# Performance work log

Hardware: AMD Instinct MI355X
Metric: run time of the kernel (lower is better)

The kernel has to match this reference:

```python
import jax, jax.numpy as jnp
import numpy as np


def _gelu(x):
    # torch nn.GELU default = exact erf form
    return jax.nn.gelu(x, approximate=False)


def setup_inputs() -> dict:
    key = jax.random.key(0)
    ks = jax.random.split(key, 10)
    B, C, S, L, Din, Dout = 32, 4, 256, 256, 256, 256
    return {
        "features": jax.random.normal(ks[0], (B, C, S, Din), jnp.float32),
        "features_mean": jax.random.normal(ks[1], (B, S, L), jnp.float32),
        "W1": jax.random.normal(ks[2], (1, 16), jnp.float32) * 0.5,
        "b1": jax.random.normal(ks[3], (16,), jnp.float32) * 0.1,
        "W2": jax.random.normal(ks[4], (16, 8), jnp.float32) * 0.25,
        "b2": jax.random.normal(ks[5], (8,), jnp.float32) * 0.1,
        "W3": jax.random.normal(ks[6], (8, 2), jnp.float32) * 0.35,
        "b3": jax.random.normal(ks[7], (2,), jnp.float32) * 0.1,
        "Wl": jax.random.normal(ks[8], (Din, Dout), jnp.float32) * (1.0 / np.sqrt(Din)),
        "bl": jax.random.normal(ks[9], (Dout,), jnp.float32) * 0.02,
    }


def reference(features, features_mean, W1, b1, W2, b2, W3, b3, Wl, bl):
    B, S, L = features_mean.shape
    # pairwise correlations -> [B, S*S, 1]
    corr = jnp.einsum('bsl,btl->bst', features_mean, features_mean).reshape(B, S * S, 1)
    # tiny pointwise MLP 1->16->8->2 with GELU, then log-softmax
    h = _gelu(corr @ W1 + b1)
    h = _gelu(h @ W2 + b2)
    logits = jax.nn.log_softmax(h @ W3 + b3, axis=-1)  # [B, S*S, 2]
    # gumbel-softmax, hard=True, tau=1 (straight-through; forward value is one-hot)
    u = jax.random.uniform(jax.random.key(42), logits.shape, logits.dtype, 1e-10, 1.0)
    g = -jnp.log(-jnp.log(u))
    y_soft = jax.nn.softmax(logits + g, axis=-1)
    y_hard = jax.nn.one_hot(jnp.argmax(y_soft, axis=-1), 2, dtype=y_soft.dtype)
    y = jax.lax.stop_gradient(y_hard - y_soft) + y_soft
    adj = y[..., 0].reshape(B, S, S)
    # mix in identity: a + (1 - a) * I (forces self-loops)
    eye = jnp.eye(S, dtype=adj.dtype)
    adj = adj + (1.0 - adj) * eye
    # degree (row) normalization
    adj = adj * (1.0 / jnp.sum(adj, axis=-1, keepdims=True))
    # propagate: [B,1,S,S] @ [B,C,S,Din]
    x = jnp.einsum('bst,bctd->bcsd', adj, features)
    return x @ Wl + bl
```

## Files before the change

### kernel.cpp

```cpp
#include <hip/hip_runtime.h>
#include <stdint.h>


#define TBL_INTERVALS 131072
#define TBL_MIN -128.0f
#define TBL_SCALE 512.0f
#define WL_CAP 131072u

typedef __attribute__((ext_vector_type(8))) short short8v;
typedef __attribute__((ext_vector_type(4))) short short4v;
typedef __attribute__((ext_vector_type(4))) float float4v;

__device__ __forceinline__ void threefry2x32(uint32_t x0, uint32_t x1,
                                             uint32_t& o0, uint32_t& o1) {
  const uint32_t ks0 = 0u;
  const uint32_t ks1 = 42u;
  const uint32_t ks2 = 0x1BD11BDAu ^ ks0 ^ ks1;
  const uint32_t ks[3] = {ks0, ks1, ks2};
  const uint32_t rot[2][4] = {{13u, 15u, 26u, 6u}, {17u, 29u, 16u, 24u}};
  x0 += ks0;
  x1 += ks1;
#pragma unroll
  for (int i = 0; i < 5; ++i) {
#pragma unroll
    for (int j = 0; j < 4; ++j) {
      const uint32_t r = rot[i & 1][j];
      x0 += x1;
      x1 = (x1 << r) | (x1 >> (32u - r));
      x1 ^= x0;
    }
    x0 += ks[(i + 1) % 3];
    x1 += ks[(i + 2) % 3] + (uint32_t)(i + 1);
  }
  o0 = x0;
  o1 = x1;
}

__device__ __forceinline__ float uniform_at(uint32_t j) {
  uint32_t o0, o1;
  threefry2x32(0u, j, o0, o1);
  const uint32_t bits = o0 ^ o1;
  uint32_t fb = (bits >> 9) | 0x3F800000u;
  float frac = __uint_as_float(fb) - 1.0f;
  return fmaxf(frac + 1e-10f, 1e-10f);
}

__device__ __forceinline__ double gumbel64_at(uint32_t j) {
  double t = -log((double)uniform_at(j));
  return -log(t);
}

__device__ __forceinline__ float gumbel32_at(uint32_t j) {
  float t = -logf(uniform_at(j));
  return -logf(t);
}

__device__ __forceinline__ double gelu_d(double x) {
  return 0.5 * x * (1.0 + erf(x * 0.70710678118654752440));
}

__device__ __forceinline__ float gelu_f(float x) {
  return 0.5f * x * (1.0f + erff(x * 0.70710678f));
}

__device__ __forceinline__ float mlp32(float corr, const float* __restrict__ W1,
                                       const float* __restrict__ b1,
                                       const float* __restrict__ W2,
                                       const float* __restrict__ b2,
                                       const float* __restrict__ W3,
                                       const float* __restrict__ b3) {
  float h1[16];
#pragma unroll
  for (int u = 0; u < 16; ++u) h1[u] = gelu_f(fmaf(corr, W1[u], b1[u]));
  float h2[8];
#pragma unroll
  for (int v = 0; v < 8; ++v) {
    float x = b2[v];
#pragma unroll
    for (int u = 0; u < 16; ++u) x = fmaf(h1[u], W2[u * 8 + v], x);
    h2[v] = gelu_f(x);
  }
  float l0 = b3[0], l1 = b3[1];
#pragma unroll
  for (int v = 0; v < 8; ++v) {
    l0 = fmaf(h2[v], W3[v * 2 + 0], l0);
    l1 = fmaf(h2[v], W3[v * 2 + 1], l1);
  }
  return l0 - l1;
}

__device__ __forceinline__ void split_bf16(float x, short& h, short& l) {
  uint32_t u = __float_as_uint(x);
  uint32_t hr = (u + 0x7FFFu + ((u >> 16) & 1u)) >> 16;
  float hf = __uint_as_float(hr << 16);
  float lo = x - hf;
  uint32_t v = __float_as_uint(lo);
  uint32_t lr = (v + 0x7FFFu + ((v >> 16) & 1u)) >> 16;
  h = (short)hr;
  l = (short)lr;
}

__global__ __launch_bounds__(256) void build_table_kernel(
    const float* __restrict__ W1, const float* __restrict__ b1,
    const float* __restrict__ W2, const float* __restrict__ b2,
    const float* __restrict__ W3, const float* __restrict__ b3,
    float* __restrict__ tbl, uint32_t* __restrict__ counter) {
  const int i = blockIdx.x * 256 + threadIdx.x;
  if (i == 0) counter[0] = 0u;
  if (i > TBL_INTERVALS) return;
  const float x = TBL_MIN + (float)i * (1.0f / TBL_SCALE);
  tbl[i] = mlp32(x, W1, b1, W2, b2, W3, b3);
}

__global__ __launch_bounds__(256) void corr_mfma_kernel(
    const float* __restrict__ fm, float* __restrict__ corr) {
  const int b = blockIdx.z;
  const float* base = fm + (size_t)b * 65536;
  const int row0 = blockIdx.y * 128;
  const int col0 = blockIdx.x * 128;

  __shared__ short Ah[128][40];
  __shared__ short Al[128][40];
  __shared__ short Bh[128][40];
  __shared__ short Bl[128][40];

  const int tid = threadIdx.x;
  const int w = tid >> 6;
  const int wr = (w >> 1) * 64;
  const int wc = (w & 1) * 64;
  const int lane = tid & 63;
  const int fcol = lane & 15;
  const int kg = lane >> 4;

  const int am = tid >> 1;
  const int ak = (tid & 1) * 16;

  float4v acc[4][4];
#pragma unroll
  for (int i = 0; i < 4; ++i)
#pragma unroll
    for (int j = 0; j < 4; ++j) acc[i][j] = (float4v)(0.0f);

  for (int k0 = 0; k0 < 256; k0 += 32) {
    float4 av[4], bv[4];
#pragma unroll
    for (int q = 0; q < 4; ++q) {
      av[q] = *(const float4*)(base + (size_t)(row0 + am) * 256 + k0 + ak + q * 4);
      bv[q] = *(const float4*)(base + (size_t)(col0 + am) * 256 + k0 + ak + q * 4);
    }

    __syncthreads();

    {
      short h[16], l[16];
#pragma unroll
      for (int q = 0; q < 4; ++q) {
        split_bf16(av[q].x, h[q * 4 + 0], l[q * 4 + 0]);
        split_bf16(av[q].y, h[q * 4 + 1], l[q * 4 + 1]);
        split_bf16(av[q].z, h[q * 4 + 2], l[q * 4 + 2]);
        split_bf16(av[q].w, h[q * 4 + 3], l[q * 4 + 3]);
      }
      *(short8v*)&Ah[am][ak] = *(short8v*)&h[0];
      *(short8v*)&Ah[am][ak + 8] = *(short8v*)&h[8];
      *(short8v*)&Al[am][ak] = *(short8v*)&l[0];
      *(short8v*)&Al[am][ak + 8] = *(short8v*)&l[8];
#pragma unroll
      for (int q = 0; q < 4; ++q) {
        split_bf16(bv[q].x, h[q * 4 + 0], l[q * 4 + 0]);
        split_bf16(bv[q].y, h[q * 4 + 1], l[q * 4 + 1]);
        split_bf16(bv[q].z, h[q * 4 + 2], l[q * 4 + 2]);
        split_bf16(bv[q].w, h[q * 4 + 3], l[q * 4 + 3]);
      }
      *(short8v*)&Bh[am][ak] = *(short8v*)&h[0];
      *(short8v*)&Bh[am][ak + 8] = *(short8v*)&h[8];
      *(short8v*)&Bl[am][ak] = *(short8v*)&l[0];
      *(short8v*)&Bl[am][ak + 8] = *(short8v*)&l[8];
    }
    __syncthreads();

    short8v afh[4], afl[4], bfh[4], bfl[4];
#pragma unroll
    for (int im = 0; im < 4; ++im) {
      afh[im] = *(const short8v*)&Ah[wr + im * 16 + fcol][kg * 8];
      afl[im] = *(const short8v*)&Al[wr + im * 16 + fcol][kg * 8];
    }
#pragma unroll
    for (int in = 0; in < 4; ++in) {
      bfh[in] = *(const short8v*)&Bh[wc + in * 16 + fcol][kg * 8];
      bfl[in] = *(const short8v*)&Bl[wc + in * 16 + fcol][kg * 8];
    }
#pragma unroll
    for (int im = 0; im < 4; ++im)
#pragma unroll
      for (int in = 0; in < 4; ++in) {
        acc[im][in] = __builtin_amdgcn_mfma_f32_16x16x32_bf16(
            afh[im], bfh[in], acc[im][in], 0, 0, 0);
        acc[im][in] = __builtin_amdgcn_mfma_f32_16x16x32_bf16(
            afh[im], bfl[in], acc[im][in], 0, 0, 0);
        acc[im][in] = __builtin_amdgcn_mfma_f32_16x16x32_bf16(
            afl[im], bfh[in], acc[im][in], 0, 0, 0);
        acc[im][in] = __builtin_amdgcn_mfma_f32_16x16x32_bf16(
            afl[im], bfl[in], acc[im][in], 0, 0, 0);
      }
  }

  float* Cb = corr + (size_t)b * 65536;
#pragma unroll
  for (int in = 0; in < 4; ++in) {
    const int col = col0 + wc + in * 16 + fcol;
#pragma unroll
    for (int im = 0; im < 4; ++im) {
      const int rbase = row0 + wr + im * 16 + kg * 4;
#pragma unroll
      for (int r = 0; r < 4; ++r)
        Cb[(size_t)(rbase + r) * 256 + col] = acc[im][in][r];
    }
  }
}

__global__ __launch_bounds__(256) void decide_fast_kernel(
    const float* __restrict__ corr, const float* __restrict__ tbl,
    unsigned short* __restrict__ adj_bin, uint32_t* __restrict__ counter,
    uint32_t* __restrict__ worklist, float* __restrict__ rowsumF) {
  const uint32_t flat = blockIdx.x * 256u + threadIdx.x;
  const int t = threadIdx.x;
  const int s = blockIdx.x & 255;

  float a = 1.0f;
  bool pend = false;
  if (t != s) {
    const float cf = corr[flat];
    if (fabsf(cf) >= 127.0f) {
      pend = true;
      a = 0.0f;
    } else {
      const float xf = (cf - TBL_MIN) * TBL_SCALE;
      const int i = (int)xf;
      const float fr = xf - (float)i;
      const float t0v = tbl[i];
      const float t1v = tbl[i + 1];
      const float dt = t1v - t0v;
      const float dphi = fmaf(fr, dt, t0v);

      const float g0 = gumbel32_at(2u * flat);
      const float g1 = gumbel32_at(2u * flat + 1u);
      const float d = dphi - (g1 - g0);
      const float thr = fmaf(fabsf(dt), 0.3072f, 4e-4f);
      if (fabsf(d) >= thr) {
        a = (d >= 0.0f) ? 1.0f : 0.0f;
      } else {
        pend = true;
        a = 0.0f;
      }
    }
  }
  if (pend) {
    const uint32_t idx = atomicAdd(counter, 1u);
    if (idx < WL_CAP) worklist[idx] = flat;
  }
  adj_bin[flat] = (a == 1.0f) ? (unsigned short)0x3F80u : (unsigned short)0u;

  float sum = a;
#pragma unroll
  for (int off = 32; off; off >>= 1) sum += __shfl_xor(sum, off);
  __shared__ float red[4];
  if ((threadIdx.x & 63) == 0) red[threadIdx.x >> 6] = sum;
  __syncthreads();
  if (threadIdx.x == 0)
    rowsumF[blockIdx.x] = red[0] + red[1] + red[2] + red[3];
}

__global__ __launch_bounds__(256) void decide_exact_kernel(
    const float* __restrict__ fm, const uint32_t* __restrict__ counter,
    const uint32_t* __restrict__ worklist,
    const float* __restrict__ W1, const float* __restrict__ b1,
    const float* __restrict__ W2, const float* __restrict__ b2,
    const float* __restrict__ W3, const float* __restrict__ b3,
    unsigned short* __restrict__ adj_bin, float* __restrict__ rowsumF) {
  const uint32_t n = min(counter[0], WL_CAP);
  const uint32_t waveId = (blockIdx.x * 256u + threadIdx.x) >> 6;
  const uint32_t nWaves = (gridDim.x * 256u) >> 6;
  const int lane = threadIdx.x & 63;

  for (uint32_t it = waveId; it < n; it += nWaves) {
    const uint32_t flat = worklist[it];
    const uint32_t bb = flat >> 16;
    const uint32_t ss = (flat >> 8) & 255u;
    const uint32_t tt = flat & 255u;

    const float* S = fm + ((size_t)bb * 256 + ss) * 256;
    const float* T = fm + ((size_t)bb * 256 + tt) * 256;
    double p = 0.0;
#pragma unroll
    for (int q = 0; q < 4; ++q) {
      const int k = lane + q * 64;
      p += (double)S[k] * (double)T[k];
    }
#pragma unroll
    for (int off = 32; off; off >>= 1) p += __shfl_xor(p, off);
    const double acc = p;

    const double ga = gumbel64_at(2u * flat + (uint32_t)(lane & 1));

    const int u = lane & 15;
    const double h1 = gelu_d(acc * (double)W1[u] + (double)b1[u]);

    const int v = lane & 7;
    double sv = (double)b2[v];
#pragma unroll
    for (int uu = 0; uu < 16; ++uu) {
      const double h1u = __shfl(h1, uu);
      sv += h1u * (double)W2[uu * 8 + v];
    }
    const double h2 = gelu_d(sv);

    double l0 = (double)b3[0], l1 = (double)b3[1];
#pragma unroll
    for (int vv = 0; vv < 8; ++vv) {
      const double h2v = __shfl(h2, vv);
      l0 += h2v * (double)W3[vv * 2 + 0];
      l1 += h2v * (double)W3[vv * 2 + 1];
    }

    const double G0 = __shfl(ga, 0);
    const double G1 = __shfl(ga, 1);
    if (lane == 0) {
      const bool one = (l0 + G0 >= l1 + G1);
      adj_bin[flat] = one ? (unsigned short)0x3F80u : (unsigned short)0u;
      if (one) atomicAdd(&rowsumF[flat >> 8], 1.0f);
    }
  }
}

__global__ __launch_bounds__(256) void gemm_binA_kernel(
    const unsigned short* __restrict__ A, const float* __restrict__ B,
    const float* __restrict__ rowsumF, float* __restrict__ C) {
  const int z = blockIdx.z;
  const unsigned short* Ab = A + (size_t)(z / 4) * 65536;
  const float* Bb = B + (size_t)z * 65536;
  const float* rsb = rowsumF + (size_t)(z / 4) * 256;
  float* Cb = C + (size_t)z * 65536;

  const int row0 = blockIdx.y * 128;
  const int col0 = blockIdx.x * 128;

  __shared__ short Ah[128][40];
  __shared__ short Bh[128][40];
  __shared__ short Bl[128][40];

  const int tid = threadIdx.x;
  const int w = tid >> 6;
  const int wr = (w >> 1) * 64;
  const int wc = (w & 1) * 64;
  const int lane = tid & 63;
  const int fcol = lane & 15;
  const int kg = lane >> 4;

  const int am = tid >> 1;
  const int ak = (tid & 1) * 16;
  const int nq = (tid & 31) * 4;
  const int kb = (tid >> 5) * 4;

  float4v acc[4][4];
#pragma unroll
  for (int i = 0; i < 4; ++i)
#pragma unroll
    for (int j = 0; j < 4; ++j) acc[i][j] = (float4v)(0.0f);

  for (int k0 = 0; k0 < 256; k0 += 32) {
    short8v a0 = *(const short8v*)(Ab + (size_t)(row0 + am) * 256 + k0 + ak);
    short8v a1 = *(const short8v*)(Ab + (size_t)(row0 + am) * 256 + k0 + ak + 8);
    float4 bv[4];
#pragma unroll
    for (int j = 0; j < 4; ++j)
      bv[j] = *(const float4*)(Bb + (size_t)(k0 + kb + j) * 256 + col0 + nq);

    __syncthreads();

    *(short8v*)&Ah[am][ak] = a0;
    *(short8v*)&Ah[am][ak + 8] = a1;
    {
      const float bm[4][4] = {{bv[0].x, bv[1].x, bv[2].x, bv[3].x},
                              {bv[0].y, bv[1].y, bv[2].y, bv[3].y},
                              {bv[0].z, bv[1].z, bv[2].z, bv[3].z},
                              {bv[0].w, bv[1].w, bv[2].w, bv[3].w}};
#pragma unroll
      for (int i = 0; i < 4; ++i) {
        short h[4], l[4];
#pragma unroll
        for (int j = 0; j < 4; ++j) split_bf16(bm[i][j], h[j], l[j]);
        *(short4v*)&Bh[nq + i][kb] = *(short4v*)&h[0];
        *(short4v*)&Bl[nq + i][kb] = *(short4v*)&l[0];
      }
    }
    __syncthreads();

    short8v afh[4], bfh[4], bfl[4];
#pragma unroll
    for (int im = 0; im < 4; ++im)
      afh[im] = *(const short8v*)&Ah[wr + im * 16 + fcol][kg * 8];
#pragma unroll
    for (int in = 0; in < 4; ++in) {
      bfh[in] = *(const short8v*)&Bh[wc + in * 16 + fcol][kg * 8];
      bfl[in] = *(const short8v*)&Bl[wc + in * 16 + fcol][kg * 8];
    }
#pragma unroll
    for (int im = 0; im < 4; ++im)
#pragma unroll
      for (int in = 0; in < 4; ++in) {
        acc[im][in] = __builtin_amdgcn_mfma_f32_16x16x32_bf16(
            afh[im], bfh[in], acc[im][in], 0, 0, 0);
        acc[im][in] = __builtin_amdgcn_mfma_f32_16x16x32_bf16(
            afh[im], bfl[in], acc[im][in], 0, 0, 0);
      }
  }

#pragma unroll
  for (int im = 0; im < 4; ++im) {
    const int rbase = row0 + wr + im * 16 + kg * 4;
    float rsv[4];
#pragma unroll
    for (int r = 0; r < 4; ++r) rsv[r] = 1.0f / rsb[rbase + r];
#pragma unroll
    for (int in = 0; in < 4; ++in) {
      const int col = col0 + wc + in * 16 + fcol;
#pragma unroll
      for (int r = 0; r < 4; ++r)
        Cb[(size_t)(rbase + r) * 256 + col] = acc[im][in][r] * rsv[r];
    }
  }
}

__global__ __launch_bounds__(256) void gemm_mfma_kernel(
    const float* __restrict__ A, const float* __restrict__ B,
    const float* __restrict__ bias, float* __restrict__ C) {
  const int z = blockIdx.z;
  const float* Ab = A + (size_t)z * 65536;
  const float* Bb = B;
  float* Cb = C + (size_t)z * 65536;

  const int row0 = blockIdx.y * 128;
  const int col0 = blockIdx.x * 128;

  __shared__ short Ah[128][40];
  __shared__ short Al[128][40];
  __shared__ short Bh[128][40];
  __shared__ short Bl[128][40];

  const int tid = threadIdx.x;
  const int w = tid >> 6;
  const int wr = (w >> 1) * 64;
  const int wc = (w & 1) * 64;
  const int lane = tid & 63;
  const int fcol = lane & 15;
  const int kg = lane >> 4;

  const int am = tid >> 1;
  const int ak = (tid & 1) * 16;
  const int nq = (tid & 31) * 4;
  const int kb = (tid >> 5) * 4;

  float4v acc[4][4];
#pragma unroll
  for (int i = 0; i < 4; ++i)
#pragma unroll
    for (int j = 0; j < 4; ++j) acc[i][j] = (float4v)(0.0f);

  for (int k0 = 0; k0 < 256; k0 += 32) {
    float4 av[4];
#pragma unroll
    for (int q = 0; q < 4; ++q)
      av[q] = *(const float4*)(Ab + (size_t)(row0 + am) * 256 + k0 + ak + q * 4);
    float4 bv[4];
#pragma unroll
    for (int j = 0; j < 4; ++j)
      bv[j] = *(const float4*)(Bb + (size_t)(k0 + kb + j) * 256 + col0 + nq);

    __syncthreads();

    {
      short h[16], l[16];
#pragma unroll
      for (int q = 0; q < 4; ++q) {
        split_bf16(av[q].x, h[q * 4 + 0], l[q * 4 + 0]);
        split_bf16(av[q].y, h[q * 4 + 1], l[q * 4 + 1]);
        split_bf16(av[q].z, h[q * 4 + 2], l[q * 4 + 2]);
        split_bf16(av[q].w, h[q * 4 + 3], l[q * 4 + 3]);
      }
      *(short8v*)&Ah[am][ak] = *(short8v*)&h[0];
      *(short8v*)&Ah[am][ak + 8] = *(short8v*)&h[8];
      *(short8v*)&Al[am][ak] = *(short8v*)&l[0];
      *(short8v*)&Al[am][ak + 8] = *(short8v*)&l[8];
    }
    {
      const float bm[4][4] = {{bv[0].x, bv[1].x, bv[2].x, bv[3].x},
                              {bv[0].y, bv[1].y, bv[2].y, bv[3].y},
                              {bv[0].z, bv[1].z, bv[2].z, bv[3].z},
                              {bv[0].w, bv[1].w, bv[2].w, bv[3].w}};
#pragma unroll
      for (int i = 0; i < 4; ++i) {
        short h[4], l[4];
#pragma unroll
        for (int j = 0; j < 4; ++j) split_bf16(bm[i][j], h[j], l[j]);
        *(short4v*)&Bh[nq + i][kb] = *(short4v*)&h[0];
        *(short4v*)&Bl[nq + i][kb] = *(short4v*)&l[0];
      }
    }
    __syncthreads();

    short8v afh[4], afl[4], bfh[4], bfl[4];
#pragma unroll
    for (int im = 0; im < 4; ++im) {
      afh[im] = *(const short8v*)&Ah[wr + im * 16 + fcol][kg * 8];
      afl[im] = *(const short8v*)&Al[wr + im * 16 + fcol][kg * 8];
    }
#pragma unroll
    for (int in = 0; in < 4; ++in) {
      bfh[in] = *(const short8v*)&Bh[wc + in * 16 + fcol][kg * 8];
      bfl[in] = *(const short8v*)&Bl[wc + in * 16 + fcol][kg * 8];
    }
#pragma unroll
    for (int im = 0; im < 4; ++im)
#pragma unroll
      for (int in = 0; in < 4; ++in) {
        acc[im][in] = __builtin_amdgcn_mfma_f32_16x16x32_bf16(
            afh[im], bfh[in], acc[im][in], 0, 0, 0);
        acc[im][in] = __builtin_amdgcn_mfma_f32_16x16x32_bf16(
            afh[im], bfl[in], acc[im][in], 0, 0, 0);
        acc[im][in] = __builtin_amdgcn_mfma_f32_16x16x32_bf16(
            afl[im], bfh[in], acc[im][in], 0, 0, 0);
      }
  }

#pragma unroll
  for (int in = 0; in < 4; ++in) {
    const int col = col0 + wc + in * 16 + fcol;
    const float bvx = bias[col];
#pragma unroll
    for (int im = 0; im < 4; ++im) {
      const int rbase = row0 + wr + im * 16 + kg * 4;
#pragma unroll
      for (int r = 0; r < 4; ++r)
        Cb[(size_t)(rbase + r) * 256 + col] = acc[im][in][r] + bvx;
    }
  }
}

extern "C" void kernel_launch(void* const* d_in, const int* in_sizes, int n_in,
                              void* d_out, int out_size, void* d_ws,
                              size_t ws_size, hipStream_t stream) {
  const float* features = (const float*)d_in[0];
  const float* fm       = (const float*)d_in[1];
  const float* W1 = (const float*)d_in[2];
  const float* b1 = (const float*)d_in[3];
  const float* W2 = (const float*)d_in[4];
  const float* b2 = (const float*)d_in[5];
  const float* W3 = (const float*)d_in[6];
  const float* b3 = (const float*)d_in[7];
  const float* Wl = (const float*)d_in[8];
  const float* bl = (const float*)d_in[9];
  float* out = (float*)d_out;

  char* ws = (char*)d_ws;
  float* tbl          = (float*)ws;
  float* rowsumF      = (float*)(ws + 576u * 1024u);
  uint32_t* counter   = (uint32_t*)(ws + 640u * 1024u);
  uint32_t* worklist  = counter + 16;
  unsigned short* adj = (unsigned short*)(ws + 2u * 1024u * 1024u);
  float* corr         = (float*)(ws + 10800u * 1024u);
  float* X            = (float*)(ws + 10800u * 1024u);

  build_table_kernel<<<dim3(513), 256, 0, stream>>>(W1, b1, W2, b2, W3, b3,
                                                    tbl, counter);
  corr_mfma_kernel<<<dim3(2, 2, 32), 256, 0, stream>>>(fm, corr);
  decide_fast_kernel<<<dim3(8192), 256, 0, stream>>>(corr, tbl, adj, counter,
                                                     worklist, rowsumF);
  decide_exact_kernel<<<dim3(2048), 256, 0, stream>>>(fm, counter, worklist,
                                                      W1, b1, W2, b2, W3, b3,
                                                      adj, rowsumF);
  gemm_binA_kernel<<<dim3(2, 2, 128), 256, 0, stream>>>(adj, features,
                                                        rowsumF, X);
  gemm_mfma_kernel<<<dim3(2, 2, 128), 256, 0, stream>>>(X, Wl, bl, out);
}
```

Measured before the change: 94.08 us.

## Fuse adjacency propagation GEMM with output linear GEMM; merge table build into corr kernel

Replaces the two back-to-back GEMM kernels with one kernel. Each block computes a 32-row strip of adj@features, keeps the normalized result in LDS as a bf16 hi/lo pair, then multiplies it by Wl, so the intermediate X never goes to global memory. The table-build kernel is also folded into the correlation kernel as extra blocks, which removes one launch. In exchange each block needs about 73KB of dynamic LDS, which lowers occupancy. The smaller 32-row tiles also mean every block re-reads full feature and Wl panels, adding redundant global traffic and repeated bf16 splitting.

```diff
diff --git a/kernel.cpp b/kernel.cpp
--- a/kernel.cpp
+++ b/kernel.cpp
@@ -6,6 +6,7 @@
 #define TBL_MIN -128.0f
 #define TBL_SCALE 512.0f
 #define WL_CAP 131072u
+#define FUSED_LDS 74752
 
 typedef __attribute__((ext_vector_type(8))) short short8v;
 typedef __attribute__((ext_vector_type(4))) short short4v;
@@ -100,24 +101,27 @@
   l = (short)lr;
 }
 
-__global__ __launch_bounds__(256) void build_table_kernel(
+__global__ __launch_bounds__(256) void corr_table_kernel(
+    const float* __restrict__ fm, float* __restrict__ corr,
     const float* __restrict__ W1, const float* __restrict__ b1,
     const float* __restrict__ W2, const float* __restrict__ b2,
     const float* __restrict__ W3, const float* __restrict__ b3,
     float* __restrict__ tbl, uint32_t* __restrict__ counter) {
-  const int i = blockIdx.x * 256 + threadIdx.x;
-  if (i == 0) counter[0] = 0u;
-  if (i > TBL_INTERVALS) return;
-  const float x = TBL_MIN + (float)i * (1.0f / TBL_SCALE);
-  tbl[i] = mlp32(x, W1, b1, W2, b2, W3, b3);
-}
-
-__global__ __launch_bounds__(256) void corr_mfma_kernel(
-    const float* __restrict__ fm, float* __restrict__ corr) {
-  const int b = blockIdx.z;
+  if (blockIdx.x >= 128) {
+    const int i = (int)(blockIdx.x - 128) * 256 + threadIdx.x;
+    if (blockIdx.x == 128 && threadIdx.x == 0) counter[0] = 0u;
+    if (i <= TBL_INTERVALS) {
+      const float x = TBL_MIN + (float)i * (1.0f / TBL_SCALE);
+      tbl[i] = mlp32(x, W1, b1, W2, b2, W3, b3);
+    }
+    return;
+  }
+
+  const int bid = blockIdx.x;
+  const int b = bid >> 2;
+  const int row0 = ((bid >> 1) & 1) * 128;
+  const int col0 = (bid & 1) * 128;
   const float* base = fm + (size_t)b * 65536;
-  const int row0 = blockIdx.y * 128;
-  const int col0 = blockIdx.x * 128;
 
   __shared__ short Ah[128][40];
   __shared__ short Al[128][40];
@@ -332,216 +336,184 @@
   }
 }
 
-__global__ __launch_bounds__(256) void gemm_binA_kernel(
-    const unsigned short* __restrict__ A, const float* __restrict__ B,
-    const float* __restrict__ rowsumF, float* __restrict__ C) {
-  const int z = blockIdx.z;
-  const unsigned short* Ab = A + (size_t)(z / 4) * 65536;
-  const float* Bb = B + (size_t)z * 65536;
-  const float* rsb = rowsumF + (size_t)(z / 4) * 256;
-  float* Cb = C + (size_t)z * 65536;
-
-  const int row0 = blockIdx.y * 128;
-  const int col0 = blockIdx.x * 128;
-
-  __shared__ short Ah[128][40];
-  __shared__ short Bh[128][40];
-  __shared__ short Bl[128][40];
+__global__ __launch_bounds__(256) void fused_out_kernel(
+    const unsigned short* __restrict__ adjp, const float* __restrict__ F,
+    const float* __restrict__ Wl, const float* __restrict__ bl,
+    const float* __restrict__ rowsumF, float* __restrict__ out) {
+  extern __shared__ char smem[];
+  short* Aadj = (short*)smem;
+  short* Xh = (short*)smem;
+  short* Xl = Xh + 32 * 264;
+  short* Bh = (short*)(smem + 33792);
+  short* Bl = Bh + 256 * 40;
+
+  const int bid = blockIdx.x;
+  const int z = bid & 127;
+  const int rg = bid >> 7;
+  const int b = z >> 2;
+  const int row0 = rg * 32;
+
+  const unsigned short* Ab = adjp + (size_t)b * 65536 + (size_t)row0 * 256;
+  const float* Fb = F + (size_t)z * 65536;
+  const float* rsb = rowsumF + b * 256 + row0;
+  float* Ob = out + (size_t)z * 65536 + (size_t)row0 * 256;
 
   const int tid = threadIdx.x;
   const int w = tid >> 6;
-  const int wr = (w >> 1) * 64;
-  const int wc = (w & 1) * 64;
+  const int wc2 = w * 64;
   const int lane = tid & 63;
   const int fcol = lane & 15;
   const int kg = lane >> 4;
 
-  const int am = tid >> 1;
-  const int ak = (tid & 1) * 16;
-  const int nq = (tid & 31) * 4;
+  const int nq = (tid & 31) * 8;
   const int kb = (tid >> 5) * 4;
 
-  float4v acc[4][4];
-#pragma unroll
-  for (int i = 0; i < 4; ++i)
+  {
+    const int r = tid >> 3;
+    const int c0 = (tid & 7) * 32;
+#pragma unroll
+    for (int q = 0; q < 4; ++q) {
+      short8v v = *(const short8v*)(Ab + (size_t)r * 256 + c0 + q * 8);
+      *(short8v*)&Aadj[r * 264 + c0 + q * 8] = v;
+    }
+  }
+
+  float4v acc[2][4];
+#pragma unroll
+  for (int i = 0; i < 2; ++i)
 #pragma unroll
     for (int j = 0; j < 4; ++j) acc[i][j] = (float4v)(0.0f);
 
   for (int k0 = 0; k0 < 256; k0 += 32) {
-    short8v a0 = *(const short8v*)(Ab + (size_t)(row0 + am) * 256 + k0 + ak);
-    short8v a1 = *(const short8v*)(Ab + (size_t)(row0 + am) * 256 + k0 + ak + 8);
-    float4 bv[4];
-#pragma unroll
-    for (int j = 0; j < 4; ++j)
-      bv[j] = *(const float4*)(Bb + (size_t)(k0 + kb + j) * 256 + col0 + nq);
-
+    float4 bv[4][2];
+#pragma unroll
+    for (int j = 0; j < 4; ++j) {
+      bv[j][0] = *(const float4*)(Fb + (size_t)(k0 + kb + j) * 256 + nq);
+      bv[j][1] = *(const float4*)(Fb + (size_t)(k0 + kb + j) * 256 + nq + 4);
+    }
     __syncthreads();
-
-    *(short8v*)&Ah[am][ak] = a0;
-    *(short8v*)&Ah[am][ak + 8] = a1;
-    {
-      const float bm[4][4] = {{bv[0].x, bv[1].x, bv[2].x, bv[3].x},
-                              {bv[0].y, bv[1].y, bv[2].y, bv[3].y},
-                              {bv[0].z, bv[1].z, bv[2].z, bv[3].z},
-                              {bv[0].w, bv[1].w, bv[2].w, bv[3].w}};
-#pragma unroll
-      for (int i = 0; i < 4; ++i) {
-        short h[4], l[4];
-#pragma unroll
-        for (int j = 0; j < 4; ++j) split_bf16(bm[i][j], h[j], l[j]);
-        *(short4v*)&Bh[nq + i][kb] = *(short4v*)&h[0];
-        *(short4v*)&Bl[nq + i][kb] = *(short4v*)&l[0];
-      }
+#pragma unroll
+    for (int i = 0; i < 8; ++i) {
+      short h[4], l[4];
+#pragma unroll
+      for (int j = 0; j < 4; ++j) {
+        const float4& f = bv[j][i >> 2];
+        const float x = ((i & 3) == 0) ? f.x
+                       : ((i & 3) == 1) ? f.y
+                       : ((i & 3) == 2) ? f.z : f.w;
+        split_bf16(x, h[j], l[j]);
+      }
+      *(short4v*)&Bh[(nq + i) * 40 + kb] = *(short4v*)&h[0];
+      *(short4v*)&Bl[(nq + i) * 40 + kb] = *(short4v*)&l[0];
     }
     __syncthreads();
 
-    short8v afh[4], bfh[4], bfl[4];
-#pragma unroll
-    for (int im = 0; im < 4; ++im)
-      afh[im] = *(const short8v*)&Ah[wr + im * 16 + fcol][kg * 8];
+    short8v af[2], bfh[4], bfl[4];
+#pragma unroll
+    for (int im = 0; im < 2; ++im)
+      af[im] = *(const short8v*)&Aadj[(im * 16 + fcol) * 264 + k0 + kg * 8];
 #pragma unroll
     for (int in = 0; in < 4; ++in) {
-      bfh[in] = *(const short8v*)&Bh[wc + in * 16 + fcol][kg * 8];
-      bfl[in] = *(const short8v*)&Bl[wc + in * 16 + fcol][kg * 8];
-    }
-#pragma unroll
-    for (int im = 0; im < 4; ++im)
+      bfh[in] = *(const short8v*)&Bh[(wc2 + in * 16 + fcol) * 40 + kg * 8];
+      bfl[in] = *(const short8v*)&Bl[(wc2 + in * 16 + fcol) * 40 + kg * 8];
+    }
+#pragma unroll
+    for (int im = 0; im < 2; ++im)
 #pragma unroll
       for (int in = 0; in < 4; ++in) {
         acc[im][in] = __builtin_amdgcn_mfma_f32_16x16x32_bf16(
+            af[im], bfh[in], acc[im][in], 0, 0, 0);
+        acc[im][in] = __builtin_amdgcn_mfma_f32_16x16x32_bf16(
+            af[im], bfl[in], acc[im][in], 0, 0, 0);
+      }
+  }
+
+  __syncthreads();
+  {
+    float rsv[2][4];
+#pragma unroll
+    for (int im = 0; im < 2; ++im)
+#pragma unroll
+      for (int r = 0; r < 4; ++r)
+        rsv[im][r] = 1.0f / rsb[im * 16 + kg * 4 + r];
+#pragma unroll
+    for (int im = 0; im < 2; ++im)
+#pragma unroll
+      for (int in = 0; in < 4; ++in) {
+        const int col = wc2 + in * 16 + fcol;
+#pragma unroll
+        for (int r = 0; r < 4; ++r) {
+          const int row = im * 16 + kg * 4 + r;
+          short h, l;
+          split_bf16(acc[im][in][r] * rsv[im][r], h, l);
+          Xh[row * 264 + col] = h;
+          Xl[row * 264 + col] = l;
+        }
+      }
+  }
+#pragma unroll
+  for (int i = 0; i < 2; ++i)
+#pragma unroll
+    for (int j = 0; j < 4; ++j) acc[i][j] = (float4v)(0.0f);
+
+  for (int k0 = 0; k0 < 256; k0 += 32) {
+    float4 bv[4][2];
+#pragma unroll
+    for (int j = 0; j < 4; ++j) {
+      bv[j][0] = *(const float4*)(Wl + (size_t)(k0 + kb + j) * 256 + nq);
+      bv[j][1] = *(const float4*)(Wl + (size_t)(k0 + kb + j) * 256 + nq + 4);
+    }
+    __syncthreads();
+#pragma unroll
+    for (int i = 0; i < 8; ++i) {
+      short h[4], l[4];
+#pragma unroll
+      for (int j = 0; j < 4; ++j) {
+        const float4& f = bv[j][i >> 2];
+        const float x = ((i & 3) == 0) ? f.x
+                       : ((i & 3) == 1) ? f.y
+                       : ((i & 3) == 2) ? f.z : f.w;
+        split_bf16(x, h[j], l[j]);
+      }
+      *(short4v*)&Bh[(nq + i) * 40 + kb] = *(short4v*)&h[0];
+      *(short4v*)&Bl[(nq + i) * 40 + kb] = *(short4v*)&l[0];
+    }
+    __syncthreads();
+
+    short8v afh[2], afl[2], bfh[4], bfl[4];
+#pragma unroll
+    for (int im = 0; im < 2; ++im) {
+      afh[im] = *(const short8v*)&Xh[(im * 16 + fcol) * 264 + k0 + kg * 8];
+      afl[im] = *(const short8v*)&Xl[(im * 16 + fcol) * 264 + k0 + kg * 8];
+    }
+#pragma unroll
+    for (int in = 0; in < 4; ++in) {
+      bfh[in] = *(const short8v*)&Bh[(wc2 + in * 16 + fcol) * 40 + kg * 8];
+      bfl[in] = *(const short8v*)&Bl[(wc2 + in * 16 + fcol) * 40 + kg * 8];
+    }
+#pragma unroll
+    for (int im = 0; im < 2; ++im)
+#pragma unroll
+      for (int in = 0; in < 4; ++in) {
+        acc[im][in] = __builtin_amdgcn_mfma_f32_16x16x32_bf16(
             afh[im], bfh[in], acc[im][in], 0, 0, 0);
         acc[im][in] = __builtin_amdgcn_mfma_f32_16x16x32_bf16(
             afh[im], bfl[in], acc[im][in], 0, 0, 0);
-      }
-  }
-
-#pragma unroll
-  for (int im = 0; im < 4; ++im) {
-    const int rbase = row0 + wr + im * 16 + kg * 4;
-    float rsv[4];
-#pragma unroll
-    for (int r = 0; r < 4; ++r) rsv[r] = 1.0f / rsb[rbase + r];
-#pragma unroll
-    for (int in = 0; in < 4; ++in) {
-      const int col = col0 + wc + in * 16 + fcol;
+        acc[im][in] = __builtin_amdgcn_mfma_f32_16x16x32_bf16(
+            afl[im], bfh[in], acc[im][in], 0, 0, 0);
+      }
+  }
+
+#pragma unroll
+  for (int in = 0; in < 4; ++in) {
+    const int col = wc2 + in * 16 + fcol;
+    const float bvx = bl[col];
+#pragma unroll
+    for (int im = 0; im < 2; ++im) {
+      const int rbase = im * 16 + kg * 4;
 #pragma unroll
       for (int r = 0; r < 4; ++r)
-        Cb[(size_t)(rbase + r) * 256 + col] = acc[im][in][r] * rsv[r];
-    }
-  }
-}
-
-__global__ __launch_bounds__(256) void gemm_mfma_kernel(
-    const float* __restrict__ A, const float* __restrict__ B,
-    const float* __restrict__ bias, float* __restrict__ C) {
-  const int z = blockIdx.z;
-  const float* Ab = A + (size_t)z * 65536;
-  const float* Bb = B;
-  float* Cb = C + (size_t)z * 65536;
-
-  const int row0 = blockIdx.y * 128;
-  const int col0 = blockIdx.x * 128;
-
-  __shared__ short Ah[128][40];
-  __shared__ short Al[128][40];
-  __shared__ short Bh[128][40];
-  __shared__ short Bl[128][40];
-
-  const int tid = threadIdx.x;
-  const int w = tid >> 6;
-  const int wr = (w >> 1) * 64;
-  const int wc = (w & 1) * 64;
-  const int lane = tid & 63;
-  const int fcol = lane & 15;
-  const int kg = lane >> 4;
-
-  const int am = tid >> 1;
-  const int ak = (tid & 1) * 16;
-  const int nq = (tid & 31) * 4;
-  const int kb = (tid >> 5) * 4;
-
-  float4v acc[4][4];
-#pragma unroll
-  for (int i = 0; i < 4; ++i)
-#pragma unroll
-    for (int j = 0; j < 4; ++j) acc[i][j] = (float4v)(0.0f);
-
-  for (int k0 = 0; k0 < 256; k0 += 32) {
-    float4 av[4];
-#pragma unroll
-    for (int q = 0; q < 4; ++q)
-      av[q] = *(const float4*)(Ab + (size_t)(row0 + am) * 256 + k0 + ak + q * 4);
-    float4 bv[4];
-#pragma unroll
-    for (int j = 0; j < 4; ++j)
-      bv[j] = *(const float4*)(Bb + (size_t)(k0 + kb + j) * 256 + col0 + nq);
-
-    __syncthreads();
-
-    {
-      short h[16], l[16];
-#pragma unroll
-      for (int q = 0; q < 4; ++q) {
-        split_bf16(av[q].x, h[q * 4 + 0], l[q * 4 + 0]);
-        split_bf16(av[q].y, h[q * 4 + 1], l[q * 4 + 1]);
-        split_bf16(av[q].z, h[q * 4 + 2], l[q * 4 + 2]);
-        split_bf16(av[q].w, h[q * 4 + 3], l[q * 4 + 3]);
-      }
-      *(short8v*)&Ah[am][ak] = *(short8v*)&h[0];
-      *(short8v*)&Ah[am][ak + 8] = *(short8v*)&h[8];
-      *(short8v*)&Al[am][ak] = *(short8v*)&l[0];
-      *(short8v*)&Al[am][ak + 8] = *(short8v*)&l[8];
-    }
-    {
-      const float bm[4][4] = {{bv[0].x, bv[1].x, bv[2].x, bv[3].x},
-                              {bv[0].y, bv[1].y, bv[2].y, bv[3].y},
-                              {bv[0].z, bv[1].z, bv[2].z, bv[3].z},
-                              {bv[0].w, bv[1].w, bv[2].w, bv[3].w}};
-#pragma unroll
-      for (int i = 0; i < 4; ++i) {
-        short h[4], l[4];
-#pragma unroll
-        for (int j = 0; j < 4; ++j) split_bf16(bm[i][j], h[j], l[j]);
-        *(short4v*)&Bh[nq + i][kb] = *(short4v*)&h[0];
-        *(short4v*)&Bl[nq + i][kb] = *(short4v*)&l[0];
-      }
-    }
-    __syncthreads();
-
-    short8v afh[4], afl[4], bfh[4], bfl[4];
-#pragma unroll
-    for (int im = 0; im < 4; ++im) {
-      afh[im] = *(const short8v*)&Ah[wr + im * 16 + fcol][kg * 8];
-      afl[im] = *(const short8v*)&Al[wr + im * 16 + fcol][kg * 8];
-    }
-#pragma unroll
-    for (int in = 0; in < 4; ++in) {
-      bfh[in] = *(const short8v*)&Bh[wc + in * 16 + fcol][kg * 8];
-      bfl[in] = *(const short8v*)&Bl[wc + in * 16 + fcol][kg * 8];
-    }
-#pragma unroll
-    for (int im = 0; im < 4; ++im)
-#pragma unroll
-      for (int in = 0; in < 4; ++in) {
-        acc[im][in] = __builtin_amdgcn_mfma_f32_16x16x32_bf16(
-            afh[im], bfh[in], acc[im][in], 0, 0, 0);
-        acc[im][in] = __builtin_amdgcn_mfma_f32_16x16x32_bf16(
-            afh[im], bfl[in], acc[im][in], 0, 0, 0);
-        acc[im][in] = __builtin_amdgcn_mfma_f32_16x16x32_bf16(
-            afl[im], bfh[in], acc[im][in], 0, 0, 0);
-      }
-  }
-
-#pragma unroll
-  for (int in = 0; in < 4; ++in) {
-    const int col = col0 + wc + in * 16 + fcol;
-    const float bvx = bias[col];
-#pragma unroll
-    for (int im = 0; im < 4; ++im) {
-      const int rbase = row0 + wr + im * 16 + kg * 4;
-#pragma unroll
-      for (int r = 0; r < 4; ++r)
-        Cb[(size_t)(rbase + r) * 256 + col] = acc[im][in][r] + bvx;
+        Ob[(size_t)(rbase + r) * 256 + col] = acc[im][in][r] + bvx;
     }
   }
 }
@@ -568,17 +540,17 @@
   uint32_t* worklist  = counter + 16;
   unsigned short* adj = (unsigned short*)(ws + 2u * 1024u * 1024u);
   float* corr         = (float*)(ws + 10800u * 1024u);
-  float* X            = (float*)(ws + 10800u * 1024u);
-
-  build_table_kernel<<<dim3(513), 256, 0, stream>>>(W1, b1, W2, b2, W3, b3,
-                                                    tbl, counter);
-  corr_mfma_kernel<<<dim3(2, 2, 32), 256, 0, stream>>>(fm, corr);
+
+  hipFuncSetAttribute((const void*)fused_out_kernel,
+                      hipFuncAttributeMaxDynamicSharedMemorySize, FUSED_LDS);
+
+  corr_table_kernel<<<dim3(641), 256, 0, stream>>>(fm, corr, W1, b1, W2, b2,
+                                                   W3, b3, tbl, counter);
   decide_fast_kernel<<<dim3(8192), 256, 0, stream>>>(corr, tbl, adj, counter,
                                                      worklist, rowsumF);
   decide_exact_kernel<<<dim3(2048), 256, 0, stream>>>(fm, counter, worklist,
                                                       W1, b1, W2, b2, W3, b3,
                                                       adj, rowsumF);
-  gemm_binA_kernel<<<dim3(2, 2, 128), 256, 0, stream>>>(adj, features,
-                                                        rowsumF, X);
-  gemm_mfma_kernel<<<dim3(2, 2, 128), 256, 0, stream>>>(X, Wl, bl, out);
-}
+  fused_out_kernel<<<dim3(1024), 256, FUSED_LDS, stream>>>(adj, features, Wl,
+                                                           bl, rowsumF, out);
+}
```

Result: slower. 184.2 us (+95.8%).
